# Kernel tuning notes

Hardware: AMD Instinct MI355X
Metric: run time of the kernel (lower is better)

The kernel has to match this reference:

```python
import jax, jax.numpy as jnp
import numpy as np

BS, N, DEG = 2, 16384, 16
NE = N * DEG          # 262144 edges
D = 128               # node/edge feature dim
S = 4                 # number of completed blocks
EPS = 1e-6


def mlp(x, W1, b1, W2, b2):
    # MLP(in, hidden=128, out, act=SiLU, layer_norm=False)
    return jax.nn.silu(x @ W1 + b1) @ W2 + b2


def rms_norm(x, w):
    return x * jax.lax.rsqrt(jnp.mean(x * x, axis=-1, keepdims=True) + EPS) * w


def setup_inputs() -> dict:
    key = jax.random.key(0)
    ks = jax.random.split(key, 14)
    f32 = jnp.float32
    sc = 0.05
    return {
        "V": jax.random.normal(ks[0], (BS, N, D), f32),
        "E": jax.random.normal(ks[1], (BS, NE, D), f32),
        "blocks": jax.random.normal(ks[2], (S, BS, N, D), f32),
        "We1": jax.random.normal(ks[3], (3 * D, D), f32) * sc,
        "be1": jnp.zeros((D,), f32),
        "We2": jax.random.normal(ks[4], (D, D), f32) * sc,
        "be2": jnp.zeros((D,), f32),
        "Wn1": jax.random.normal(ks[5], (2 * D, D), f32) * sc,
        "bn1": jnp.zeros((D,), f32),
        "Wn2": jax.random.normal(ks[6], (D, D), f32) * sc,
        "bn2": jnp.zeros((D,), f32),
        "w_attn": jax.random.normal(ks[7], (D,), f32) * sc,
        "rms_w": jnp.ones((D,), f32),
        "edges": jax.random.randint(ks[8], (BS, NE, 2), 0, N, jnp.int32),
    }


def reference(V, E, blocks, We1, be1, We2, be2, Wn1, bn1, Wn2, bn2,
              w_attn, rms_w, edges):
    # ---- GNN layer: edge gather -> edge MLP -> scatter_mean -> node MLP ----
    senders = jnp.take_along_axis(V, edges[..., 0][:, :, None], axis=1)    # [b,E,D]
    receivers = jnp.take_along_axis(V, edges[..., 1][:, :, None], axis=1)  # [b,E,D]
    edge_inpt = jnp.concatenate([senders, receivers, E], axis=-1)          # [b,E,3D]
    edge_emb = mlp(edge_inpt, We1, be1, We2, be2)                          # [b,E,D]
    e0, e1 = jnp.split(edge_emb, 2, axis=-1)                               # [b,E,D/2] each

    def seg_mean(vals, idx):
        s = jax.ops.segment_sum(vals, idx, num_segments=N)
        c = jax.ops.segment_sum(jnp.ones(idx.shape, vals.dtype), idx,
                                num_segments=N)
        return s / jnp.maximum(c, 1.0)[:, None]

    m0 = jax.vmap(seg_mean)(e0, edges[..., 0])   # [b,N,D/2]
    m1 = jax.vmap(seg_mean)(e1, edges[..., 1])   # [b,N,D/2]
    node_inpt = jnp.concatenate([V, m0, m1], axis=-1)                      # [b,N,2D]
    node_emb = mlp(node_inpt, Wn1, bn1, Wn2, bn2)                          # [b,N,D]

    # ---- block_attn_res: depth-wise attention over stacked blocks ----
    Vs = jnp.concatenate([blocks, node_emb[None]], axis=0)                 # [S+1,b,N,D]
    K = rms_norm(Vs, rms_w)
    logits = jnp.einsum('d,sbnd->sbn', w_attn, K)
    alpha = jax.nn.softmax(logits, axis=0)
    h = jnp.einsum('sbn,sbnd->bnd', alpha, Vs)                             # [b,N,D]
    return h
```

## Files before the change

### kernel.cpp

```cpp
#include <hip/hip_runtime.h>
#include <hip/hip_bf16.h>

#define D 128
#define NNODES 16384
#define NEDGES 262144
#define NBATCH 2
#define TE 128

typedef __attribute__((ext_vector_type(8))) short bf16x8;
typedef __attribute__((ext_vector_type(4))) float f32x4;

__device__ __forceinline__ unsigned int pk2bf(float lo, float hi) {
    unsigned int r;
    asm("v_cvt_pk_bf16_f32 %0, %1, %2" : "=v"(r) : "v"(lo), "v"(hi));
    return r;
}

__device__ __forceinline__ unsigned short f2bf(float f) {
    return (unsigned short)pk2bf(f, f);
}

__device__ __forceinline__ float bflo(unsigned int u) {
    return __uint_as_float(u << 16);
}
__device__ __forceinline__ float bfhi(unsigned int u) {
    return __uint_as_float(u & 0xffff0000u);
}

__device__ __forceinline__ bf16x8 pack8(f32x4 a, f32x4 b) {
    typedef __attribute__((ext_vector_type(4))) unsigned int u32x4;
    u32x4 u;
    u.x = pk2bf(a[0], a[1]);
    u.y = pk2bf(a[2], a[3]);
    u.z = pk2bf(b[0], b[1]);
    u.w = pk2bf(b[2], b[3]);
    return __builtin_bit_cast(bf16x8, u);
}

__device__ __forceinline__ void atomic_pk(unsigned int* p, unsigned int v) {
    asm volatile("global_atomic_pk_add_bf16 %0, %1, off" :: "v"(p), "v"(v) : "memory");
}

__global__ __launch_bounds__(256)
void prep_weights(const float* __restrict__ We1, const float* __restrict__ We2,
                  const float* __restrict__ Wn1, const float* __restrict__ Wn2,
                  unsigned short* __restrict__ w)
{
    int id = blockIdx.x * 256 + threadIdx.x;
    if (id < 16384) {
        int e = id & 7, l = (id >> 3) & 63, nblk = (id >> 9) & 7, ks = id >> 12;
        int k = 256 + ks * 32 + ((l >> 4) & 3) * 8 + e;
        int col = nblk * 16 + (l & 15);
        w[id] = f2bf(We1[k * 128 + col]);
    } else if (id < 32768) {
        int i2 = id - 16384;
        int e = i2 & 7, l = (i2 >> 3) & 63, nblk = (i2 >> 9) & 7, ks = i2 >> 12;
        int k = ks * 32 + ((l >> 4) & 3) * 8 + e;
        int col = nblk * 16 + (l & 15);
        w[id] = f2bf(We2[k * 128 + col]);
    } else if (id < 65536) {
        int i3 = id - 32768;
        int j = i3 >> 7, k = i3 & 127;
        int row = (j < 128) ? k : (128 + k);
        w[id] = f2bf(We1[row * 128 + (j & 127)]);
    } else if (id < 98304) {
        int i4 = id - 65536;
        int n = i4 >> 8, k = i4 & 255;
        w[id] = f2bf(Wn1[k * 128 + n]);
    } else {
        int i5 = id - 98304;
        int n = i5 >> 7, k = i5 & 127;
        w[id] = f2bf(Wn2[k * 128 + n]);
    }
}

__global__ __launch_bounds__(256)
void partial_kernel(const float* __restrict__ V, const unsigned short* __restrict__ wp,
                    unsigned short* __restrict__ P)
{
    __shared__ unsigned short smem[64 * 136];
    const int t = threadIdx.x, lane = t & 63, wave = t >> 6;
    const int l15 = lane & 15, l4 = lane >> 4;
    const long long r0 = (long long)blockIdx.x * 64;

    for (int i = t; i < 64 * 32; i += 256) {
        int c4 = i & 31, r = i >> 5;
        float4 v = *(const float4*)(V + (r0 + r) * 128 + c4 * 4);
        uint2 p; p.x = pk2bf(v.x, v.y); p.y = pk2bf(v.z, v.w);
        *(uint2*)(&smem[r * 136 + c4 * 4]) = p;
    }
    __syncthreads();

    const int j0 = wave * 64;
    f32x4 acc[4][4] = {};
    const unsigned short* bb0 = wp + (j0 + l15) * 128 + l4 * 8;
    #pragma unroll
    for (int ks = 0; ks < 4; ++ks) {
        bf16x8 bb[4];
        #pragma unroll
        for (int n = 0; n < 4; ++n)
            bb[n] = *(const bf16x8*)(bb0 + n * 16 * 128 + ks * 32);
        #pragma unroll
        for (int mq = 0; mq < 4; ++mq) {
            bf16x8 a = *(const bf16x8*)(&smem[(mq * 16 + l15) * 136 + l4 * 8 + ks * 32]);
            #pragma unroll
            for (int n = 0; n < 4; ++n)
                acc[mq][n] = __builtin_amdgcn_mfma_f32_16x16x32_bf16(a, bb[n], acc[mq][n], 0, 0, 0);
        }
    }
    const int pbase = (wave >> 1) * 128 + (wave & 1) * 64 + l15 * 4;
    #pragma unroll
    for (int mq = 0; mq < 4; ++mq) {
        #pragma unroll
        for (int i = 0; i < 4; ++i) {
            int row = mq * 16 + l4 * 4 + i;
            uint2 pw;
            pw.x = pk2bf(acc[mq][0][i], acc[mq][1][i]);
            pw.y = pk2bf(acc[mq][2][i], acc[mq][3][i]);
            *(uint2*)(P + (r0 + row) * 256 + pbase) = pw;
        }
    }
}

__global__ __launch_bounds__(512)
void edge_kernel(const float* __restrict__ E, const int* __restrict__ edges,
                 const unsigned short* __restrict__ P,
                 const unsigned short* __restrict__ w1ef, const float* __restrict__ be1,
                 const unsigned short* __restrict__ w2f,
                 unsigned short* __restrict__ us_m0, unsigned short* __restrict__ us_m1,
                 float* __restrict__ c0, float* __restrict__ c1)
{
    __shared__ unsigned short Hbuf[TE * 136];

    const int t    = threadIdx.x;
    const int lane = t & 63;
    const int wave = t >> 6;
    const int wr   = wave >> 1;
    const int wc   = wave & 1;
    const int l15  = lane & 15;
    const int l4   = lane >> 4;

    const long long eflat0 = (long long)blockIdx.x * TE;
    const int b  = (int)(eflat0 / NEDGES);
    const long long nb0 = (long long)b * NNODES;

    if (t < TE) {
        int2 e2 = *(const int2*)(edges + (eflat0 + t) * 2);
        atomicAdd(&c0[nb0 + e2.x], 1.f);
        atomicAdd(&c1[nb0 + e2.y], 1.f);
    }

    int nd0[2][4], nd1[2][4];
    #pragma unroll
    for (int m = 0; m < 2; ++m) {
        #pragma unroll
        for (int i = 0; i < 4; ++i) {
            int row = wr * 32 + m * 16 + l4 * 4 + i;
            int2 e2 = *(const int2*)(edges + (eflat0 + row) * 2);
            nd0[m][i] = e2.x;
            nd1[m][i] = e2.y;
        }
    }

    const unsigned short* Pb = P + nb0 * 256;
    const unsigned int wcl = wc * 64 + l15 * 4;
    uint2 su[2][4], ru[2][4];
    #pragma unroll
    for (int m = 0; m < 2; ++m) {
        #pragma unroll
        for (int i = 0; i < 4; ++i) {
            su[m][i] = *(const uint2*)(Pb + (unsigned)nd0[m][i] * 256u + wcl);
            ru[m][i] = *(const uint2*)(Pb + (unsigned)nd1[m][i] * 256u + 128u + wcl);
        }
    }

    f32x4 acc[2][4] = {};
    {
        const float* er0 = E + (eflat0 + wr * 32 + l15) * D + l4 * 8;
        #pragma unroll
        for (int ks = 0; ks < 4; ++ks) {
            f32x4 xa0 = *(const f32x4*)(er0 + ks * 32);
            f32x4 xb0 = *(const f32x4*)(er0 + ks * 32 + 4);
            f32x4 xa1 = *(const f32x4*)(er0 + 16 * D + ks * 32);
            f32x4 xb1 = *(const f32x4*)(er0 + 16 * D + ks * 32 + 4);
            bf16x8 a0 = pack8(xa0, xb0);
            bf16x8 a1 = pack8(xa1, xb1);
            #pragma unroll
            for (int n = 0; n < 4; ++n) {
                bf16x8 bb = *(const bf16x8*)(w1ef + (((ks * 8 + wc * 4 + n) * 64 + lane) << 3));
                acc[0][n] = __builtin_amdgcn_mfma_f32_16x16x32_bf16(a0, bb, acc[0][n], 0, 0, 0);
                acc[1][n] = __builtin_amdgcn_mfma_f32_16x16x32_bf16(a1, bb, acc[1][n], 0, 0, 0);
            }
        }
    }

    float bia[4];
    #pragma unroll
    for (int n = 0; n < 4; ++n) bia[n] = be1[wc * 64 + n * 16 + l15];
    #pragma unroll
    for (int m = 0; m < 2; ++m) {
        #pragma unroll
        for (int i = 0; i < 4; ++i) {
            int row = wr * 32 + m * 16 + l4 * 4 + i;
            float ps[4] = { bflo(su[m][i].x), bfhi(su[m][i].x),
                            bflo(su[m][i].y), bfhi(su[m][i].y) };
            float pr[4] = { bflo(ru[m][i].x), bfhi(ru[m][i].x),
                            bflo(ru[m][i].y), bfhi(ru[m][i].y) };
            #pragma unroll
            for (int n = 0; n < 4; ++n) {
                float a = acc[m][n][i] + bia[n] + ps[n] + pr[n];
                Hbuf[row * 136 + wc * 64 + n * 16 + l15] = f2bf(a / (1.f + __expf(-a)));
            }
        }
    }
    __syncthreads();

    f32x4 acc2[2][4] = {};
    {
        const unsigned short* hrow = &Hbuf[(wr * 32 + l15) * 136 + l4 * 8];
        #pragma unroll
        for (int ks = 0; ks < 4; ++ks) {
            bf16x8 a0 = *(const bf16x8*)(hrow + ks * 32);
            bf16x8 a1 = *(const bf16x8*)(hrow + 16 * 136 + ks * 32);
            #pragma unroll
            for (int n = 0; n < 4; ++n) {
                bf16x8 bb = *(const bf16x8*)(w2f + (((ks * 8 + wc * 4 + n) * 64 + lane) << 3));
                acc2[0][n] = __builtin_amdgcn_mfma_f32_16x16x32_bf16(a0, bb, acc2[0][n], 0, 0, 0);
                acc2[1][n] = __builtin_amdgcn_mfma_f32_16x16x32_bf16(a1, bb, acc2[1][n], 0, 0, 0);
            }
        }
    }

    {
        unsigned short* dst_arr = wc ? us_m1 : us_m0;
        #pragma unroll
        for (int n = 0; n < 4; ++n) {
            int colh = n * 16 + l15;
            #pragma unroll
            for (int m = 0; m < 2; ++m) {
                #pragma unroll
                for (int i = 0; i < 4; ++i) {
                    int node = wc ? nd1[m][i] : nd0[m][i];
                    float v  = acc2[m][n][i];
                    float vn = __shfl_xor(v, 1);
                    if (!(lane & 1)) {
                        atomic_pk((unsigned int*)(dst_arr + (nb0 + node) * 64 + colh),
                                  pk2bf(v, vn));
                    }
                }
            }
        }
    }
}

__global__ __launch_bounds__(256)
void node_kernel(const float* __restrict__ V,
                 const unsigned short* __restrict__ m0, const unsigned short* __restrict__ m1,
                 const float* __restrict__ c0, const float* __restrict__ c1,
                 const float* __restrict__ be2,
                 const unsigned short* __restrict__ wn1t, const float* __restrict__ bn1,
                 const unsigned short* __restrict__ wn2t, const float* __restrict__ bn2,
                 float* __restrict__ node_emb)
{
    __shared__ unsigned short smem[64 * 264];

    const int t    = threadIdx.x;
    const int lane = t & 63;
    const int wave = t >> 6;
    const int wr   = wave >> 1;
    const int wc   = wave & 1;
    const int l15  = lane & 15;
    const int l4   = lane >> 4;

    const long long nflat0 = (long long)blockIdx.x * 64;

    for (int i = t; i < 64 * 48; i += 256) {
        int n  = i / 48;
        int c4 = i - n * 48;
        long long node = nflat0 + n;
        if (c4 < 32) {
            float4 v = *(const float4*)(V + node * 128 + c4 * 4);
            uint2 p; p.x = pk2bf(v.x, v.y); p.y = pk2bf(v.z, v.w);
            *(uint2*)(&smem[n * 264 + c4 * 4]) = p;
        } else {
            int dir = (c4 >= 40);
            int j = c4 - 32 - dir * 8;
            const unsigned short* src = dir ? m1 : m0;
            float cnt = (dir ? c1 : c0)[node];
            float inv = 1.f / fmaxf(cnt, 1.f);
            float bon = (cnt >= 1.f) ? 1.f : 0.f;
            uint4 raw = *(const uint4*)(src + node * 64 + j * 8);
            const float* bb = be2 + dir * 64 + j * 8;
            unsigned int rr[4] = {raw.x, raw.y, raw.z, raw.w};
            unsigned int o[4];
            #pragma unroll
            for (int q = 0; q < 4; ++q) {
                float lo = bflo(rr[q]) * inv + bb[2 * q] * bon;
                float hi = bfhi(rr[q]) * inv + bb[2 * q + 1] * bon;
                o[q] = pk2bf(lo, hi);
            }
            uint4 st; st.x = o[0]; st.y = o[1]; st.z = o[2]; st.w = o[3];
            *(uint4*)(&smem[n * 264 + 128 + dir * 64 + j * 8]) = st;
        }
    }
    __syncthreads();

    f32x4 acc[2][4] = {};
    {
        const unsigned short* arow = &smem[(wr * 32 + l15) * 264 + l4 * 8];
        const unsigned short* bb0  = wn1t + (wc * 64 + l15) * 256 + l4 * 8;
        for (int ks = 0; ks < 8; ++ks) {
            bf16x8 a0 = *(const bf16x8*)(arow + ks * 32);
            bf16x8 a1 = *(const bf16x8*)(arow + 16 * 264 + ks * 32);
            #pragma unroll
            for (int n = 0; n < 4; ++n) {
                bf16x8 bb = *(const bf16x8*)(bb0 + n * 16 * 256 + ks * 32);
                acc[0][n] = __builtin_amdgcn_mfma_f32_16x16x32_bf16(a0, bb, acc[0][n], 0, 0, 0);
                acc[1][n] = __builtin_amdgcn_mfma_f32_16x16x32_bf16(a1, bb, acc[1][n], 0, 0, 0);
            }
        }
    }
    __syncthreads();

    #pragma unroll
    for (int n = 0; n < 4; ++n) {
        int col = wc * 64 + n * 16 + l15;
        float bias = bn1[col];
        #pragma unroll
        for (int m = 0; m < 2; ++m) {
            #pragma unroll
            for (int i = 0; i < 4; ++i) {
                int row = wr * 32 + m * 16 + l4 * 4 + i;
                float a = acc[m][n][i] + bias;
                smem[row * 136 + col] = f2bf(a / (1.f + __expf(-a)));
            }
        }
    }
    __syncthreads();

    f32x4 acc2[2][4] = {};
    {
        const unsigned short* hrow = &smem[(wr * 32 + l15) * 136 + l4 * 8];
        const unsigned short* bb0  = wn2t + (wc * 64 + l15) * 128 + l4 * 8;
        #pragma unroll
        for (int ks = 0; ks < 4; ++ks) {
            bf16x8 a0 = *(const bf16x8*)(hrow + ks * 32);
            bf16x8 a1 = *(const bf16x8*)(hrow + 16 * 136 + ks * 32);
            #pragma unroll
            for (int n = 0; n < 4; ++n) {
                bf16x8 bb = *(const bf16x8*)(bb0 + n * 16 * 128 + ks * 32);
                acc2[0][n] = __builtin_amdgcn_mfma_f32_16x16x32_bf16(a0, bb, acc2[0][n], 0, 0, 0);
                acc2[1][n] = __builtin_amdgcn_mfma_f32_16x16x32_bf16(a1, bb, acc2[1][n], 0, 0, 0);
            }
        }
    }

    #pragma unroll
    for (int n = 0; n < 4; ++n) {
        int col = wc * 64 + n * 16 + l15;
        float bias = bn2[col];
        #pragma unroll
        for (int m = 0; m < 2; ++m) {
            #pragma unroll
            for (int i = 0; i < 4; ++i) {
                long long row = nflat0 + wr * 32 + m * 16 + l4 * 4 + i;
                node_emb[row * 128 + col] = acc2[m][n][i] + bias;
            }
        }
    }
}

__global__ __launch_bounds__(256)
void attn_kernel(const float* __restrict__ blocks, const float* __restrict__ node_emb,
                 const float* __restrict__ w_attn, const float* __restrict__ rms_w,
                 float* __restrict__ out)
{
    const int t    = threadIdx.x;
    const int wave = t >> 6;
    const int lane = t & 63;
    const long long node = (long long)blockIdx.x * 4 + wave;
    const int d0 = lane * 2;

    float2 wa = *(const float2*)(w_attn + d0);
    float2 rw = *(const float2*)(rms_w + d0);

    float xs[5][2];
    float lg[5];
    #pragma unroll
    for (int s = 0; s < 5; ++s) {
        const float* src = (s < 4)
            ? (blocks + ((long long)s * NBATCH * NNODES + node) * 128)
            : (node_emb + node * 128);
        float2 x = *(const float2*)(src + d0);
        xs[s][0] = x.x; xs[s][1] = x.y;
        float ss = x.x * x.x + x.y * x.y;
        float wv = wa.x * rw.x * x.x + wa.y * rw.y * x.y;
        #pragma unroll
        for (int m = 1; m < 64; m <<= 1) {
            ss += __shfl_xor(ss, m);
            wv += __shfl_xor(wv, m);
        }
        lg[s] = wv * rsqrtf(ss * (1.f / 128.f) + 1e-6f);
    }

    float mx = lg[0];
    #pragma unroll
    for (int s = 1; s < 5; ++s) mx = fmaxf(mx, lg[s]);
    float ex[5], sum = 0.f;
    #pragma unroll
    for (int s = 0; s < 5; ++s) { ex[s] = __expf(lg[s] - mx); sum += ex[s]; }
    float inv = 1.f / sum;

    float h0 = 0.f, h1 = 0.f;
    #pragma unroll
    for (int s = 0; s < 5; ++s) {
        float a = ex[s] * inv;
        h0 = fmaf(a, xs[s][0], h0);
        h1 = fmaf(a, xs[s][1], h1);
    }
    *(float2*)(out + node * 128 + d0) = make_float2(h0, h1);
}

extern "C" void kernel_launch(void* const* d_in, const int* in_sizes, int n_in,
                              void* d_out, int out_size, void* d_ws, size_t ws_size,
                              hipStream_t stream)
{
    const float* V      = (const float*)d_in[0];
    const float* E      = (const float*)d_in[1];
    const float* blocks = (const float*)d_in[2];
    const float* We1    = (const float*)d_in[3];
    const float* be1    = (const float*)d_in[4];
    const float* We2    = (const float*)d_in[5];
    const float* be2    = (const float*)d_in[6];
    const float* Wn1    = (const float*)d_in[7];
    const float* bn1    = (const float*)d_in[8];
    const float* Wn2    = (const float*)d_in[9];
    const float* bn2    = (const float*)d_in[10];
    const float* w_attn = (const float*)d_in[11];
    const float* rms_w  = (const float*)d_in[12];
    const int*   edges  = (const int*)d_in[13];
    float* out = (float*)d_out;

    unsigned short* us_m0 = (unsigned short*)d_ws;
    unsigned short* us_m1 = us_m0 + 2097152;
    float* c0       = (float*)(us_m1 + 2097152);
    float* c1       = c0 + 32768;
    float* node_emb = c1 + 32768;
    unsigned short* wbf = (unsigned short*)(node_emb + 4194304);
    unsigned short* w1ef = wbf;
    unsigned short* w2f  = wbf + 16384;
    unsigned short* wp   = wbf + 32768;
    unsigned short* wn1t = wbf + 65536;
    unsigned short* wn2t = wbf + 98304;
    unsigned short* P    = wbf + 114688;

    (void)hipMemsetAsync(d_ws, 0, (size_t)(2097152 * 2 * 2 + 32768 * 2 * 4), stream);

    prep_weights<<<448, 256, 0, stream>>>(We1, We2, Wn1, Wn2, wbf);

    partial_kernel<<<(NBATCH * NNODES) / 64, 256, 0, stream>>>(V, wp, P);

    edge_kernel<<<(NBATCH * NEDGES) / TE, 512, 0, stream>>>(
        E, edges, P, w1ef, be1, w2f, us_m0, us_m1, c0, c1);

    node_kernel<<<(NBATCH * NNODES) / 64, 256, 0, stream>>>(
        V, us_m0, us_m1, c0, c1, be2, wn1t, bn1, wn2t, bn2, node_emb);

    attn_kernel<<<(NBATCH * NNODES) / 4, 256, 0, stream>>>(
        blocks, node_emb, w_attn, rms_w, out);
}
```

Before: 361.2 us.

## Split fused edge MLP into two kernels with global bf16 hidden buffer

The single edge kernel that kept the hidden activation in shared memory is split into edge_l1 (first layer plus SiLU, written to a global bf16 buffer H) and edge_l2 (reads H, runs the second layer and scatters). Blocks shrink from 512 threads/128 edges to 256 threads/64 edges with no LDS. Edges are processed in chunks sized to the available workspace. The aim is higher occupancy and less register and LDS pressure, at the cost of an extra global round trip of about 134MB for H and more launches.

```diff
diff --git a/kernel.cpp b/kernel.cpp
--- a/kernel.cpp
+++ b/kernel.cpp
@@ -5,7 +5,6 @@
 #define NNODES 16384
 #define NEDGES 262144
 #define NBATCH 2
-#define TE 128
 
 typedef __attribute__((ext_vector_type(8))) short bf16x8;
 typedef __attribute__((ext_vector_type(4))) float f32x4;
@@ -122,16 +121,12 @@
     }
 }
 
-__global__ __launch_bounds__(512)
-void edge_kernel(const float* __restrict__ E, const int* __restrict__ edges,
-                 const unsigned short* __restrict__ P,
-                 const unsigned short* __restrict__ w1ef, const float* __restrict__ be1,
-                 const unsigned short* __restrict__ w2f,
-                 unsigned short* __restrict__ us_m0, unsigned short* __restrict__ us_m1,
-                 float* __restrict__ c0, float* __restrict__ c1)
-{
-    __shared__ unsigned short Hbuf[TE * 136];
-
+__global__ __launch_bounds__(256)
+void edge_l1(const float* __restrict__ E, const int* __restrict__ edges,
+             const unsigned short* __restrict__ P,
+             const unsigned short* __restrict__ w1ef, const float* __restrict__ be1,
+             unsigned short* __restrict__ H, long long chunk0)
+{
     const int t    = threadIdx.x;
     const int lane = t & 63;
     const int wave = t >> 6;
@@ -140,15 +135,9 @@
     const int l15  = lane & 15;
     const int l4   = lane >> 4;
 
-    const long long eflat0 = (long long)blockIdx.x * TE;
+    const long long eflat0 = chunk0 + (long long)blockIdx.x * 64;
     const int b  = (int)(eflat0 / NEDGES);
     const long long nb0 = (long long)b * NNODES;
-
-    if (t < TE) {
-        int2 e2 = *(const int2*)(edges + (eflat0 + t) * 2);
-        atomicAdd(&c0[nb0 + e2.x], 1.f);
-        atomicAdd(&c1[nb0 + e2.y], 1.f);
-    }
 
     int nd0[2][4], nd1[2][4];
     #pragma unroll
@@ -201,7 +190,7 @@
     for (int m = 0; m < 2; ++m) {
         #pragma unroll
         for (int i = 0; i < 4; ++i) {
-            int row = wr * 32 + m * 16 + l4 * 4 + i;
+            long long lrow = (long long)blockIdx.x * 64 + wr * 32 + m * 16 + l4 * 4 + i;
             float ps[4] = { bflo(su[m][i].x), bfhi(su[m][i].x),
                             bflo(su[m][i].y), bfhi(su[m][i].y) };
             float pr[4] = { bflo(ru[m][i].x), bfhi(ru[m][i].x),
@@ -209,19 +198,61 @@
             #pragma unroll
             for (int n = 0; n < 4; ++n) {
                 float a = acc[m][n][i] + bia[n] + ps[n] + pr[n];
-                Hbuf[row * 136 + wc * 64 + n * 16 + l15] = f2bf(a / (1.f + __expf(-a)));
-            }
-        }
-    }
-    __syncthreads();
+                float hv = a / (1.f + __expf(-a));
+                float hn = __shfl_xor(hv, 1);
+                if (!(lane & 1)) {
+                    *(unsigned int*)(H + lrow * 128 + wc * 64 + n * 16 + l15) =
+                        pk2bf(hv, hn);
+                }
+            }
+        }
+    }
+}
+
+__global__ __launch_bounds__(256)
+void edge_l2(const unsigned short* __restrict__ H, const int* __restrict__ edges,
+             const unsigned short* __restrict__ w2f,
+             unsigned short* __restrict__ us_m0, unsigned short* __restrict__ us_m1,
+             float* __restrict__ c0, float* __restrict__ c1, long long chunk0)
+{
+    const int t    = threadIdx.x;
+    const int lane = t & 63;
+    const int wave = t >> 6;
+    const int wr   = wave >> 1;
+    const int wc   = wave & 1;
+    const int l15  = lane & 15;
+    const int l4   = lane >> 4;
+
+    const long long eflat0 = chunk0 + (long long)blockIdx.x * 64;
+    const int b  = (int)(eflat0 / NEDGES);
+    const long long nb0 = (long long)b * NNODES;
+
+    if (t < 64) {
+        int2 e2 = *(const int2*)(edges + (eflat0 + t) * 2);
+        atomicAdd(&c0[nb0 + e2.x], 1.f);
+        atomicAdd(&c1[nb0 + e2.y], 1.f);
+    }
+
+    int nd0[2][4], nd1[2][4];
+    #pragma unroll
+    for (int m = 0; m < 2; ++m) {
+        #pragma unroll
+        for (int i = 0; i < 4; ++i) {
+            int row = wr * 32 + m * 16 + l4 * 4 + i;
+            int2 e2 = *(const int2*)(edges + (eflat0 + row) * 2);
+            nd0[m][i] = e2.x;
+            nd1[m][i] = e2.y;
+        }
+    }
 
     f32x4 acc2[2][4] = {};
     {
-        const unsigned short* hrow = &Hbuf[(wr * 32 + l15) * 136 + l4 * 8];
+        const unsigned short* hrow =
+            H + ((long long)blockIdx.x * 64 + wr * 32 + l15) * 128 + l4 * 8;
         #pragma unroll
         for (int ks = 0; ks < 4; ++ks) {
             bf16x8 a0 = *(const bf16x8*)(hrow + ks * 32);
-            bf16x8 a1 = *(const bf16x8*)(hrow + 16 * 136 + ks * 32);
+            bf16x8 a1 = *(const bf16x8*)(hrow + 16 * 128 + ks * 32);
             #pragma unroll
             for (int n = 0; n < 4; ++n) {
                 bf16x8 bb = *(const bf16x8*)(w2f + (((ks * 8 + wc * 4 + n) * 64 + lane) << 3));
@@ -443,16 +474,26 @@
 
     unsigned short* us_m0 = (unsigned short*)d_ws;
     unsigned short* us_m1 = us_m0 + 2097152;
-    float* c0       = (float*)(us_m1 + 2097152);
-    float* c1       = c0 + 32768;
-    float* node_emb = c1 + 32768;
-    unsigned short* wbf = (unsigned short*)(node_emb + 4194304);
+    float* c0 = (float*)(us_m1 + 2097152);
+    float* c1 = c0 + 32768;
+    unsigned short* wbf = (unsigned short*)(c1 + 32768);
     unsigned short* w1ef = wbf;
     unsigned short* w2f  = wbf + 16384;
     unsigned short* wp   = wbf + 32768;
     unsigned short* wn1t = wbf + 65536;
     unsigned short* wn2t = wbf + 98304;
     unsigned short* P    = wbf + 114688;
+    float* node_emb = (float*)(P + 8388608);
+    unsigned short* H = (unsigned short*)node_emb;
+
+    const size_t head = (size_t)((char*)node_emb - (char*)d_ws);
+    const size_t hfull = (size_t)NBATCH * NEDGES * 128 * 2;
+    const size_t ne_bytes = (size_t)NBATCH * NNODES * 128 * 4;
+    int nch;
+    if      (head + (hfull     > ne_bytes ? hfull     : ne_bytes) <= ws_size) nch = 1;
+    else if (head + (hfull / 2 > ne_bytes ? hfull / 2 : ne_bytes) <= ws_size) nch = 2;
+    else if (head + (hfull / 4 > ne_bytes ? hfull / 4 : ne_bytes) <= ws_size) nch = 4;
+    else nch = 8;
 
     (void)hipMemsetAsync(d_ws, 0, (size_t)(2097152 * 2 * 2 + 32768 * 2 * 4), stream);
 
@@ -460,8 +501,13 @@
 
     partial_kernel<<<(NBATCH * NNODES) / 64, 256, 0, stream>>>(V, wp, P);
 
-    edge_kernel<<<(NBATCH * NEDGES) / TE, 512, 0, stream>>>(
-        E, edges, P, w1ef, be1, w2f, us_m0, us_m1, c0, c1);
+    const long long epc = (long long)NBATCH * NEDGES / nch;
+    for (int ci = 0; ci < nch; ++ci) {
+        long long chunk0 = ci * epc;
+        edge_l1<<<(int)(epc / 64), 256, 0, stream>>>(E, edges, P, w1ef, be1, H, chunk0);
+        edge_l2<<<(int)(epc / 64), 256, 0, stream>>>(H, edges, w2f, us_m0, us_m1,
+                                                     c0, c1, chunk0);
+    }
 
     node_kernel<<<(NBATCH * NNODES) / 64, 256, 0, stream>>>(
         V, us_m0, us_m1, c0, c1, be2, wn1t, bn1, wn2t, bn2, node_emb);
```

Result: slower. 489.1 us (+35.4%).

## Replace bf16 atomic scatter-mean with CSR sort and deterministic gather reduction

Applied to the files above, without the earlier changes.

Replaces the per-edge packed bf16 global atomics for the scatter-mean with a counting sort: count, scan and fill kernels build per-node CSR edge lists. The edge kernel now writes per-edge embeddings densely to a staging buffer, one batch at a time. A gather kernel then sums each node's edges in fp32 and applies the mean and bias. This removes atomic contention and bf16 accumulation error, but adds several kernel launches, a 64MB-per-batch round trip of edge embeddings through memory, and atomics in the fill step.

```diff
diff --git a/kernel.cpp b/kernel.cpp
--- a/kernel.cpp
+++ b/kernel.cpp
@@ -35,10 +35,6 @@
     u.z = pk2bf(b[0], b[1]);
     u.w = pk2bf(b[2], b[3]);
     return __builtin_bit_cast(bf16x8, u);
-}
-
-__device__ __forceinline__ void atomic_pk(unsigned int* p, unsigned int v) {
-    asm volatile("global_atomic_pk_add_bf16 %0, %1, off" :: "v"(p), "v"(v) : "memory");
 }
 
 __global__ __launch_bounds__(256)
@@ -122,13 +118,67 @@
     }
 }
 
+__global__ __launch_bounds__(256)
+void count_kernel(const int* __restrict__ edges, int* __restrict__ cnt)
+{
+    int id = blockIdx.x * 256 + threadIdx.x;
+    int b = id >> 18;
+    int2 e = ((const int2*)edges)[id];
+    atomicAdd(&cnt[(b << 14) + e.x], 1);
+    atomicAdd(&cnt[32768 + (b << 14) + e.y], 1);
+}
+
+__global__ __launch_bounds__(1024)
+void scan_kernel(const int* __restrict__ cnt, int* __restrict__ off, int* __restrict__ cur)
+{
+    __shared__ int part[1024];
+    const int a = blockIdx.x;
+    const int t = threadIdx.x;
+    const int* c = cnt + a * 32768;
+    int* o  = off + a * 32768;
+    int* cu = cur + a * 32768;
+    int base = t * 32;
+    int loc[32];
+    int s = 0;
+    #pragma unroll
+    for (int i = 0; i < 32; ++i) { loc[i] = s; s += c[base + i]; }
+    part[t] = s;
+    __syncthreads();
+    for (int d = 1; d < 1024; d <<= 1) {
+        int v = (t >= d) ? part[t - d] : 0;
+        __syncthreads();
+        part[t] += v;
+        __syncthreads();
+    }
+    int pre = (t == 0) ? 0 : part[t - 1];
+    #pragma unroll
+    for (int i = 0; i < 32; ++i) {
+        int v = pre + loc[i];
+        o[base + i]  = v;
+        cu[base + i] = v;
+    }
+}
+
+__global__ __launch_bounds__(256)
+void fill_kernel(const int* __restrict__ edges, int* __restrict__ cur,
+                 int* __restrict__ idx)
+{
+    int id = blockIdx.x * 256 + threadIdx.x;
+    int b = id >> 18;
+    int2 e = ((const int2*)edges)[id];
+    int p0 = atomicAdd(&cur[(b << 14) + e.x], 1);
+    idx[p0] = id;
+    int p1 = atomicAdd(&cur[32768 + (b << 14) + e.y], 1);
+    idx[NBATCH * NEDGES + p1] = id;
+}
+
 __global__ __launch_bounds__(512)
 void edge_kernel(const float* __restrict__ E, const int* __restrict__ edges,
                  const unsigned short* __restrict__ P,
                  const unsigned short* __restrict__ w1ef, const float* __restrict__ be1,
                  const unsigned short* __restrict__ w2f,
-                 unsigned short* __restrict__ us_m0, unsigned short* __restrict__ us_m1,
-                 float* __restrict__ c0, float* __restrict__ c1)
+                 unsigned short* __restrict__ out0, unsigned short* __restrict__ out1,
+                 long long chunk0)
 {
     __shared__ unsigned short Hbuf[TE * 136];
 
@@ -140,15 +190,9 @@
     const int l15  = lane & 15;
     const int l4   = lane >> 4;
 
-    const long long eflat0 = (long long)blockIdx.x * TE;
+    const long long eflat0 = chunk0 + (long long)blockIdx.x * TE;
     const int b  = (int)(eflat0 / NEDGES);
     const long long nb0 = (long long)b * NNODES;
-
-    if (t < TE) {
-        int2 e2 = *(const int2*)(edges + (eflat0 + t) * 2);
-        atomicAdd(&c0[nb0 + e2.x], 1.f);
-        atomicAdd(&c1[nb0 + e2.y], 1.f);
-    }
 
     int nd0[2][4], nd1[2][4];
     #pragma unroll
@@ -232,7 +276,7 @@
     }
 
     {
-        unsigned short* dst_arr = wc ? us_m1 : us_m0;
+        unsigned short* dst = wc ? out1 : out0;
         #pragma unroll
         for (int n = 0; n < 4; ++n) {
             int colh = n * 16 + l15;
@@ -240,12 +284,11 @@
             for (int m = 0; m < 2; ++m) {
                 #pragma unroll
                 for (int i = 0; i < 4; ++i) {
-                    int node = wc ? nd1[m][i] : nd0[m][i];
+                    long long lrow = (long long)blockIdx.x * TE + wr * 32 + m * 16 + l4 * 4 + i;
                     float v  = acc2[m][n][i];
                     float vn = __shfl_xor(v, 1);
                     if (!(lane & 1)) {
-                        atomic_pk((unsigned int*)(dst_arr + (nb0 + node) * 64 + colh),
-                                  pk2bf(v, vn));
+                        *(unsigned int*)(dst + lrow * 64 + colh) = pk2bf(v, vn);
                     }
                 }
             }
@@ -254,10 +297,48 @@
 }
 
 __global__ __launch_bounds__(256)
+void gather_kernel(const unsigned short* __restrict__ out0,
+                   const unsigned short* __restrict__ out1,
+                   const int* __restrict__ idx, const int* __restrict__ off,
+                   const int* __restrict__ cnt, const float* __restrict__ be2,
+                   unsigned short* __restrict__ m0, unsigned short* __restrict__ m1,
+                   int batch)
+{
+    const int t = threadIdx.x;
+    const int grp = t >> 4, l = t & 15;
+    int gid = blockIdx.x * 16 + grp;
+    int dir = gid >> 14;
+    int n   = gid & 16383;
+    int nf  = (batch << 14) + n;
+
+    int o = off[dir * 32768 + nf];
+    int c = cnt[dir * 32768 + nf];
+    const unsigned short* src = dir ? out1 : out0;
+    const int* ix = idx + (long long)dir * (NBATCH * NEDGES);
+
+    float a0 = 0.f, a1 = 0.f, a2 = 0.f, a3 = 0.f;
+    for (int j = 0; j < c; ++j) {
+        int eid = ix[o + j] - batch * NEDGES;
+        uint2 v = *(const uint2*)(src + (long long)eid * 64 + l * 4);
+        a0 += bflo(v.x); a1 += bfhi(v.x);
+        a2 += bflo(v.y); a3 += bfhi(v.y);
+    }
+    float inv  = (c > 0) ? (1.f / (float)c) : 0.f;
+    float gate = (c > 0) ? 1.f : 0.f;
+    const float* bb = be2 + dir * 64 + l * 4;
+    a0 = a0 * inv + bb[0] * gate;
+    a1 = a1 * inv + bb[1] * gate;
+    a2 = a2 * inv + bb[2] * gate;
+    a3 = a3 * inv + bb[3] * gate;
+    uint2 w;
+    w.x = pk2bf(a0, a1);
+    w.y = pk2bf(a2, a3);
+    *(uint2*)((dir ? m1 : m0) + (long long)nf * 64 + l * 4) = w;
+}
+
+__global__ __launch_bounds__(256)
 void node_kernel(const float* __restrict__ V,
                  const unsigned short* __restrict__ m0, const unsigned short* __restrict__ m1,
-                 const float* __restrict__ c0, const float* __restrict__ c1,
-                 const float* __restrict__ be2,
                  const unsigned short* __restrict__ wn1t, const float* __restrict__ bn1,
                  const unsigned short* __restrict__ wn2t, const float* __restrict__ bn2,
                  float* __restrict__ node_emb)
@@ -286,21 +367,8 @@
             int dir = (c4 >= 40);
             int j = c4 - 32 - dir * 8;
             const unsigned short* src = dir ? m1 : m0;
-            float cnt = (dir ? c1 : c0)[node];
-            float inv = 1.f / fmaxf(cnt, 1.f);
-            float bon = (cnt >= 1.f) ? 1.f : 0.f;
             uint4 raw = *(const uint4*)(src + node * 64 + j * 8);
-            const float* bb = be2 + dir * 64 + j * 8;
-            unsigned int rr[4] = {raw.x, raw.y, raw.z, raw.w};
-            unsigned int o[4];
-            #pragma unroll
-            for (int q = 0; q < 4; ++q) {
-                float lo = bflo(rr[q]) * inv + bb[2 * q] * bon;
-                float hi = bfhi(rr[q]) * inv + bb[2 * q + 1] * bon;
-                o[q] = pk2bf(lo, hi);
-            }
-            uint4 st; st.x = o[0]; st.y = o[1]; st.z = o[2]; st.w = o[3];
-            *(uint4*)(&smem[n * 264 + 128 + dir * 64 + j * 8]) = st;
+            *(uint4*)(&smem[n * 264 + 128 + dir * 64 + j * 8]) = raw;
         }
     }
     __syncthreads();
@@ -441,30 +509,42 @@
     const int*   edges  = (const int*)d_in[13];
     float* out = (float*)d_out;
 
-    unsigned short* us_m0 = (unsigned short*)d_ws;
-    unsigned short* us_m1 = us_m0 + 2097152;
-    float* c0       = (float*)(us_m1 + 2097152);
-    float* c1       = c0 + 32768;
-    float* node_emb = c1 + 32768;
-    unsigned short* wbf = (unsigned short*)(node_emb + 4194304);
+    int* cnti = (int*)d_ws;
+    int* cur  = cnti + 65536;
+    int* offi = cur + 65536;
+    int* idx  = offi + 65536;
+    unsigned short* m0  = (unsigned short*)(idx + 2 * NBATCH * NEDGES / 2 * 2);
+    unsigned short* m1  = m0 + 2097152;
+    unsigned short* wbf = m1 + 2097152;
     unsigned short* w1ef = wbf;
     unsigned short* w2f  = wbf + 16384;
     unsigned short* wp   = wbf + 32768;
     unsigned short* wn1t = wbf + 65536;
     unsigned short* wn2t = wbf + 98304;
     unsigned short* P    = wbf + 114688;
-
-    (void)hipMemsetAsync(d_ws, 0, (size_t)(2097152 * 2 * 2 + 32768 * 2 * 4), stream);
+    unsigned short* out0 = P + 8388608;
+    unsigned short* out1 = out0 + (size_t)NEDGES * 64;
+    float* node_emb = (float*)(out1 + (size_t)NEDGES * 64);
+
+    (void)hipMemsetAsync(cnti, 0, 65536 * sizeof(int), stream);
 
     prep_weights<<<448, 256, 0, stream>>>(We1, We2, Wn1, Wn2, wbf);
 
     partial_kernel<<<(NBATCH * NNODES) / 64, 256, 0, stream>>>(V, wp, P);
 
-    edge_kernel<<<(NBATCH * NEDGES) / TE, 512, 0, stream>>>(
-        E, edges, P, w1ef, be1, w2f, us_m0, us_m1, c0, c1);
+    count_kernel<<<(NBATCH * NEDGES) / 256, 256, 0, stream>>>(edges, cnti);
+    scan_kernel<<<2, 1024, 0, stream>>>(cnti, offi, cur);
+    fill_kernel<<<(NBATCH * NEDGES) / 256, 256, 0, stream>>>(edges, cur, idx);
+
+    for (int b = 0; b < NBATCH; ++b) {
+        edge_kernel<<<NEDGES / TE, 512, 0, stream>>>(
+            E, edges, P, w1ef, be1, w2f, out0, out1, (long long)b * NEDGES);
+        gather_kernel<<<2048, 256, 0, stream>>>(
+            out0, out1, idx, offi, cnti, be2, m0, m1, b);
+    }
 
     node_kernel<<<(NBATCH * NNODES) / 64, 256, 0, stream>>>(
-        V, us_m0, us_m1, c0, c1, be2, wn1t, bn1, wn2t, bn2, node_emb);
+        V, m0, m1, wn1t, bn1, wn2t, bn2, node_emb);
 
     attn_kernel<<<(NBATCH * NNODES) / 4, 256, 0, stream>>>(
         blocks, node_emb, w_attn, rms_w, out);
```

Measured after the change: 388.9 us. +7.7%, slower.
